# Kernel tuning notes

Hardware: AMD Instinct MI355X
Metric: run time of the kernel (lower is better)

Reference implementation:

```python
import jax, jax.numpy as jnp
import numpy as np

B, P, D, S = 1024, 200, 512, 64  # batch, num prototypes (nall), feat_dim, subdim


def setup_inputs() -> dict:
    key = jax.random.key(0)
    k1, k2, k3 = jax.random.split(key, 3)
    x = jax.random.normal(k1, (B, D), dtype=jnp.float32)
    protos = jax.random.normal(k2, (P, D), dtype=jnp.float32)
    subspaces = jax.random.normal(k3, (P, D, S), dtype=jnp.float32)
    return {"x": x, "protos": protos, "subspaces": subspaces}


def reference(x, protos, subspaces):
    # diff: [B, P, D]
    diff = x[:, None, :] - protos[None, :, :]
    # per-prototype tangent-space projectors: I - U U^T, [P, D, D]
    projectors = jnp.eye(D, dtype=subspaces.dtype) - jnp.einsum(
        'pds,pes->pde', subspaces, subspaces)
    # project diffs and take L2 norm over feature dim -> [B, P]
    proj_diff = jnp.einsum('bpd,pde->bpe', diff, projectors)
    return jnp.linalg.norm(proj_diff, ord=2, axis=-1)
```

## Files before the change

kernel.cpp:

```cpp
#include <hip/hip_runtime.h>
#include <math.h>


#define NB 1024
#define NP 200
#define ND 512
#define NS 64
#define NS5 80

#define OFF_G   0
#define OFF_C   819200
#define OFF_PN  832000
#define OFF_XN  832256
#define OFF_XB  833280
#define OFF_UB  1095424

typedef __attribute__((ext_vector_type(8))) short bf16x8;
typedef __attribute__((ext_vector_type(8))) unsigned short ushort8;
typedef __attribute__((ext_vector_type(4))) float f32x4;

__device__ __forceinline__ unsigned short f2bf(float f) {
  unsigned int u = __float_as_uint(f);
  u += 0x7fffu + ((u >> 16) & 1u);
  return (unsigned short)(u >> 16);
}

__global__ __launch_bounds__(256) void k_conv_x(const float* __restrict__ x,
                                                float* __restrict__ ws) {
  const int tid = threadIdx.x, l = tid & 63, w = tid >> 6;
  const int b = blockIdx.x * 4 + w;
  const float* src = x + (size_t)b * ND + l * 8;
  float4 v0 = *(const float4*)(src);
  float4 v1 = *(const float4*)(src + 4);
  ushort8 o;
  o[0]=f2bf(v0.x); o[1]=f2bf(v0.y); o[2]=f2bf(v0.z); o[3]=f2bf(v0.w);
  o[4]=f2bf(v1.x); o[5]=f2bf(v1.y); o[6]=f2bf(v1.z); o[7]=f2bf(v1.w);
  *(ushort8*)((unsigned short*)(ws + OFF_XB) + (size_t)b * ND + l * 8) = o;
  float s = v0.x*v0.x + v0.y*v0.y + v0.z*v0.z + v0.w*v0.w
          + v1.x*v1.x + v1.y*v1.y + v1.z*v1.z + v1.w*v1.w;
#pragma unroll
  for (int m = 1; m < 64; m <<= 1) s += __shfl_xor(s, m);
  if (l == 0) ws[OFF_XN + b] = s;
}

__global__ __launch_bounds__(256) void k_conv_u(const float* __restrict__ U,
                                                float* __restrict__ ws) {
  const int d0 = blockIdx.x * 64;
  const int p  = blockIdx.y;
  __shared__ float ts[64][68];
  const int tid = threadIdx.x;
  {
    const int dd = tid >> 4, s4 = (tid & 15) << 2;
#pragma unroll
    for (int i = 0; i < 4; ++i)
      *(float4*)&ts[dd + i*16][s4] =
          *(const float4*)(U + ((size_t)p * ND + d0 + dd + i*16) * NS + s4);
  }
  __syncthreads();
  const int s = tid >> 2, j = tid & 3;
  unsigned short* dst = (unsigned short*)(ws + OFF_UB) +
                        ((size_t)p * NS5 + s) * ND + d0 + j * 16;
  ushort8 o0, o1;
#pragma unroll
  for (int i = 0; i < 8; ++i) o0[i] = f2bf(ts[j*16 + i][s]);
#pragma unroll
  for (int i = 0; i < 8; ++i) o1[i] = f2bf(ts[j*16 + 8 + i][s]);
  *(ushort8*)dst = o0;
  *(ushort8*)(dst + 8) = o1;
}

__global__ __launch_bounds__(256) void k_conv_pz(const float* __restrict__ protos,
                                                 float* __restrict__ ws) {
  const int p = blockIdx.x, tid = threadIdx.x;
  unsigned short* ub = (unsigned short*)(ws + OFF_UB);
  float2 v = *(const float2*)(protos + (size_t)p * ND + tid * 2);
  unsigned short* d64 = ub + ((size_t)p * NS5 + 64) * ND + tid * 2;
  d64[0] = f2bf(v.x); d64[1] = f2bf(v.y);
  ushort8 z = {0,0,0,0,0,0,0,0};
#pragma unroll
  for (int i = 0; i < 4; ++i) {
    int g = tid + i * 256;
    if (g < 960)
      *(ushort8*)(ub + ((size_t)p * NS5 + 65) * ND + g * 8) = z;
  }
}

__global__ __launch_bounds__(256) void k_gram(float* __restrict__ ws) {
  const int p = blockIdx.x;
  __shared__ __align__(16) unsigned short ut[NS5 * ND];
  const int tid = threadIdx.x, l = tid & 63, w = tid >> 6;
  const int lm = l & 15, lh = l >> 4;
  const unsigned short* ub =
      (const unsigned short*)(ws + OFF_UB) + (size_t)p * NS5 * ND;
#pragma unroll
  for (int i = 0; i < 20; ++i) {
    int f = tid + i * 256;
    int r = f >> 6;
    int gd = (f & 63) ^ (r & 15);
    *(ushort8*)(ut + (size_t)f * 8) = *(const ushort8*)(ub + (size_t)r * ND + gd * 8);
  }
  __syncthreads();
  const int ntile = (w == 0) ? 6 : 5;
  for (int idx = 0; idx < ntile; ++idx) {
    int tt = (idx == 5) ? 20 : (w + 4 * idx);
    int i1 = (tt == 20) ? 4 : tt / 5;
    int i2 = (tt == 20) ? 4 : tt % 5;
    f32x4 g = {0.f, 0.f, 0.f, 0.f};
#pragma unroll
    for (int ks = 0; ks < 16; ++ks) {
      int sl = (ks * 4 + lh) ^ lm;
      bf16x8 a = *(const bf16x8*)(ut + (size_t)(i1*16 + lm) * ND + sl * 8);
      bf16x8 b = *(const bf16x8*)(ut + (size_t)(i2*16 + lm) * ND + sl * 8);
      g = __builtin_amdgcn_mfma_f32_16x16x32_bf16(a, b, g, 0, 0, 0);
    }
    int col = i2 * 16 + lm;
    int row0 = i1 * 16 + lh * 4;
    if (i1 < 4 && i2 < 4) {
#pragma unroll
      for (int q = 0; q < 4; ++q)
        ws[OFF_G + (size_t)p * 4096 + (size_t)(row0 + q) * 64 + col] = g[q];
    } else if (i1 < 4 && i2 == 4 && lm == 0) {
#pragma unroll
      for (int q = 0; q < 4; ++q) ws[OFF_C + p * 64 + row0 + q] = g[q];
    } else if (tt == 20 && l == 0) {
      ws[OFF_PN + p] = g[0];
    }
  }
}

__global__ __launch_bounds__(256) void k_main(float* __restrict__ ws,
                                              float* __restrict__ out) {
  const int p = blockIdx.y;
  const int b0 = blockIdx.x * 128;
  __shared__ __align__(16) char smem[70400];
  unsigned short* xs = (unsigned short*)smem;
  unsigned short* us = (unsigned short*)(smem + 32768);
  float* tst = (float*)smem;
  float* gs  = (float*)(smem + 53248);
  float* cs  = (float*)(smem + 69632);
  float* xps = (float*)(smem + 69888);
  const int tid = threadIdx.x, l = tid & 63, w = tid >> 6;
  const int lm = l & 15, lh = l >> 4;

#pragma unroll
  for (int it = 0; it < 4; ++it) {
    int e = tid + it * 256;
    *(float4*)(gs + e * 4) = *(const float4*)(ws + OFF_G + (size_t)p * 4096 + e * 4);
  }
  if (tid < 16)
    *(float4*)(cs + tid * 4) = *(const float4*)(ws + OFF_C + p * 64 + tid * 4);

  const unsigned short* Xb = (const unsigned short*)(ws + OFF_XB) + (size_t)b0 * ND;
  const unsigned short* Ub = (const unsigned short*)(ws + OFF_UB) + (size_t)p * NS5 * ND;

  f32x4 acc[2][5] = {};
  for (int k0 = 0; k0 < ND; k0 += 128) {
#pragma unroll
    for (int i = 0; i < 8; ++i) {
      int f = tid + i * 256;
      int r = f >> 4;
      int gd = (f & 15) ^ (r & 15);
      *(ushort8*)(xs + (size_t)f * 8) =
          *(const ushort8*)(Xb + (size_t)r * ND + k0 + gd * 8);
    }
#pragma unroll
    for (int i = 0; i < 5; ++i) {
      int f = tid + i * 256;
      int r = f >> 4;
      int gd = (f & 15) ^ (r & 15);
      *(ushort8*)(us + (size_t)f * 8) =
          *(const ushort8*)(Ub + (size_t)r * ND + k0 + gd * 8);
    }
    __syncthreads();
#pragma unroll
    for (int ks = 0; ks < 4; ++ks) {
      int gsl = ((ks * 4 + lh) ^ lm) * 8;
      bf16x8 a0 = *(const bf16x8*)(xs + (size_t)((w*2+0)*16 + lm) * 128 + gsl);
      bf16x8 a1 = *(const bf16x8*)(xs + (size_t)((w*2+1)*16 + lm) * 128 + gsl);
#pragma unroll
      for (int j = 0; j < 5; ++j) {
        bf16x8 b = *(const bf16x8*)(us + (size_t)(j*16 + lm) * 128 + gsl);
        acc[0][j] = __builtin_amdgcn_mfma_f32_16x16x32_bf16(a0, b, acc[0][j], 0, 0, 0);
        acc[1][j] = __builtin_amdgcn_mfma_f32_16x16x32_bf16(a1, b, acc[1][j], 0, 0, 0);
      }
    }
    __syncthreads();
  }

#pragma unroll
  for (int i = 0; i < 2; ++i) {
    int rbase = (w * 2 + i) * 16 + lh * 4;
#pragma unroll
    for (int j = 0; j < 5; ++j) {
      f32x4 v = acc[i][j];
      if (j < 4) {
        int col = j * 16 + lm;
        float cj = cs[col];
#pragma unroll
        for (int q = 0; q < 4; ++q)
          tst[(size_t)col * 132 + rbase + q] = v[q] - cj;
      } else if (lm == 0) {
#pragma unroll
        for (int q = 0; q < 4; ++q) xps[rbase + q] = v[q];
      }
    }
  }
  __syncthreads();

  const int tx = tid & 15, ty = tid >> 4;
  float h[8][4] = {};
#pragma unroll 4
  for (int k = 0; k < 64; ++k) {
    float4 ta = *(const float4*)(tst + k * 132 + (ty << 3));
    float4 tb = *(const float4*)(tst + k * 132 + (ty << 3) + 4);
    float4 gv = *(const float4*)(gs + k * 64 + (tx << 2));
    float tr[8] = {ta.x, ta.y, ta.z, ta.w, tb.x, tb.y, tb.z, tb.w};
    float gj[4] = {gv.x, gv.y, gv.z, gv.w};
#pragma unroll
    for (int i = 0; i < 8; ++i)
#pragma unroll
      for (int j = 0; j < 4; ++j) h[i][j] += tr[i] * gj[j];
  }

  float tgt[8], tn[8];
#pragma unroll
  for (int i = 0; i < 8; ++i) { tgt[i] = 0.f; tn[i] = 0.f; }
#pragma unroll
  for (int i = 0; i < 8; ++i)
#pragma unroll
    for (int j = 0; j < 4; ++j) {
      float tv = tst[(size_t)((tx << 2) + j) * 132 + (ty << 3) + i];
      tgt[i] += h[i][j] * tv;
      tn[i] += tv * tv;
    }
#pragma unroll
  for (int m = 1; m <= 8; m <<= 1)
#pragma unroll
    for (int i = 0; i < 8; ++i) {
      tgt[i] += __shfl_xor(tgt[i], m);
      tn[i] += __shfl_xor(tn[i], m);
    }

  if (tx == 0) {
    float pnv = ws[OFF_PN + p];
#pragma unroll
    for (int i = 0; i < 8; ++i) {
      int r = (ty << 3) + i;
      int b = b0 + r;
      float q = ws[OFF_XN + b] - 2.f * xps[r] + pnv;
      float v = q - 2.f * tn[i] + tgt[i];
      out[(size_t)b * NP + p] = sqrtf(fmaxf(v, 0.f));
    }
  }
}

extern "C" void kernel_launch(void* const* d_in, const int* in_sizes, int n_in,
                              void* d_out, int out_size, void* d_ws, size_t ws_size,
                              hipStream_t stream) {
  const float* x      = (const float*)d_in[0];
  const float* protos = (const float*)d_in[1];
  const float* U      = (const float*)d_in[2];
  float* out = (float*)d_out;
  float* ws  = (float*)d_ws;

  k_conv_x <<<dim3(NB / 4),      dim3(256), 0, stream>>>(x, ws);
  k_conv_u <<<dim3(8, NP),       dim3(256), 0, stream>>>(U, ws);
  k_conv_pz<<<dim3(NP),          dim3(256), 0, stream>>>(protos, ws);
  k_gram   <<<dim3(NP),          dim3(256), 0, stream>>>(ws);
  k_main   <<<dim3(NB / 128, NP), dim3(256), 0, stream>>>(ws, out);
}
```

Measured before the change: 145.3 us.

## Fuse preprocessing kernels and move Gram correction onto bf16 MFMA

Merges the x conversion, U transpose/conversion, proto packing and Gram computation into a single k_pre launch, so U is converted once and kept in LDS for the Gram MFMAs instead of being reread from global memory. In k_main the Gram matrix is stored as bf16 and the T·G correction runs on MFMA instead of scalar FP32 FMAs. The K-tile shrinks to 64, which cuts LDS use and should allow more resident blocks. The extra rounding of T and G to bf16 adds numerical error to the norm correction term.

```diff
diff --git a/kernel.cpp b/kernel.cpp
--- a/kernel.cpp
+++ b/kernel.cpp
@@ -8,12 +8,12 @@
 #define NS 64
 #define NS5 80
 
-#define OFF_G   0
-#define OFF_C   819200
-#define OFF_PN  832000
-#define OFF_XN  832256
-#define OFF_XB  833280
-#define OFF_UB  1095424
+#define OFF_C   0
+#define OFF_PN  12800
+#define OFF_XN  13000
+#define OFF_GB  14024
+#define OFF_XB  423624
+#define OFF_UB  685768
 
 typedef __attribute__((ext_vector_type(8))) short bf16x8;
 typedef __attribute__((ext_vector_type(8))) unsigned short ushort8;
@@ -24,82 +24,87 @@
   u += 0x7fffu + ((u >> 16) & 1u);
   return (unsigned short)(u >> 16);
 }
-
-__global__ __launch_bounds__(256) void k_conv_x(const float* __restrict__ x,
-                                                float* __restrict__ ws) {
-  const int tid = threadIdx.x, l = tid & 63, w = tid >> 6;
-  const int b = blockIdx.x * 4 + w;
-  const float* src = x + (size_t)b * ND + l * 8;
-  float4 v0 = *(const float4*)(src);
-  float4 v1 = *(const float4*)(src + 4);
-  ushort8 o;
-  o[0]=f2bf(v0.x); o[1]=f2bf(v0.y); o[2]=f2bf(v0.z); o[3]=f2bf(v0.w);
-  o[4]=f2bf(v1.x); o[5]=f2bf(v1.y); o[6]=f2bf(v1.z); o[7]=f2bf(v1.w);
-  *(ushort8*)((unsigned short*)(ws + OFF_XB) + (size_t)b * ND + l * 8) = o;
-  float s = v0.x*v0.x + v0.y*v0.y + v0.z*v0.z + v0.w*v0.w
-          + v1.x*v1.x + v1.y*v1.y + v1.z*v1.z + v1.w*v1.w;
-#pragma unroll
-  for (int m = 1; m < 64; m <<= 1) s += __shfl_xor(s, m);
-  if (l == 0) ws[OFF_XN + b] = s;
-}
-
-__global__ __launch_bounds__(256) void k_conv_u(const float* __restrict__ U,
-                                                float* __restrict__ ws) {
-  const int d0 = blockIdx.x * 64;
-  const int p  = blockIdx.y;
-  __shared__ float ts[64][68];
+__device__ __forceinline__ float bf2f(unsigned short h) {
+  return __uint_as_float(((unsigned int)h) << 16);
+}
+
+__global__ __launch_bounds__(256) void k_pre(
+    const float* __restrict__ x, const float* __restrict__ protos,
+    const float* __restrict__ U, float* __restrict__ ws)
+{
+  const int bid = blockIdx.x;
   const int tid = threadIdx.x;
+  if (bid >= NP) {
+    const int b = (bid - NP) * 32 + (tid >> 3);
+    const int cc = tid & 7;
+    const float* src = x + (size_t)b * ND + cc * 64;
+    unsigned short* dst = (unsigned short*)(ws + OFF_XB) + (size_t)b * ND + cc * 64;
+    float s = 0.f;
+#pragma unroll
+    for (int i = 0; i < 8; ++i) {
+      float4 v0 = *(const float4*)(src + i * 8);
+      float4 v1 = *(const float4*)(src + i * 8 + 4);
+      ushort8 o;
+      o[0]=f2bf(v0.x); o[1]=f2bf(v0.y); o[2]=f2bf(v0.z); o[3]=f2bf(v0.w);
+      o[4]=f2bf(v1.x); o[5]=f2bf(v1.y); o[6]=f2bf(v1.z); o[7]=f2bf(v1.w);
+      *(ushort8*)(dst + i * 8) = o;
+      s += v0.x*v0.x + v0.y*v0.y + v0.z*v0.z + v0.w*v0.w
+         + v1.x*v1.x + v1.y*v1.y + v1.z*v1.z + v1.w*v1.w;
+    }
+    s += __shfl_xor(s, 1); s += __shfl_xor(s, 2); s += __shfl_xor(s, 4);
+    if (cc == 0) ws[OFF_XN + b] = s;
+    return;
+  }
+  const int p = bid;
+  __shared__ __align__(16) unsigned short ut[NS5 * ND];
+  __shared__ float ts[32][68];
+  const int l = tid & 63, w = tid >> 6;
+  const int lm = l & 15, lh = l >> 4;
+  unsigned short* Ubg = (unsigned short*)(ws + OFF_UB) + (size_t)p * NS5 * ND;
+
+  for (int ch = 0; ch < 16; ++ch) {
+    const int d0 = ch * 32;
+    {
+      const int dd = tid >> 3, c8 = (tid & 7) * 8;
+      const float* srcu = U + ((size_t)p * ND + d0 + dd) * NS + c8;
+      *(float4*)&ts[dd][c8]     = *(const float4*)(srcu);
+      *(float4*)&ts[dd][c8 + 4] = *(const float4*)(srcu + 4);
+    }
+    __syncthreads();
+    {
+      const int s = tid >> 2, jj = tid & 3;
+      ushort8 o;
+#pragma unroll
+      for (int i = 0; i < 8; ++i) o[i] = f2bf(ts[jj * 8 + i][s]);
+      const int gd = ch * 4 + jj;
+      *(ushort8*)(ut + ((size_t)s * 64 + (gd ^ (s & 15))) * 8) = o;
+      *(ushort8*)(Ubg + (size_t)s * ND + gd * 8) = o;
+    }
+    __syncthreads();
+  }
+  if (tid < 64) {
+    const float* pr = protos + (size_t)p * ND + tid * 8;
+    float4 v0 = *(const float4*)(pr);
+    float4 v1 = *(const float4*)(pr + 4);
+    ushort8 o;
+    o[0]=f2bf(v0.x); o[1]=f2bf(v0.y); o[2]=f2bf(v0.z); o[3]=f2bf(v0.w);
+    o[4]=f2bf(v1.x); o[5]=f2bf(v1.y); o[6]=f2bf(v1.z); o[7]=f2bf(v1.w);
+    *(ushort8*)(ut + ((size_t)64 * 64 + tid) * 8) = o;
+    *(ushort8*)(Ubg + (size_t)64 * ND + tid * 8) = o;
+  }
   {
-    const int dd = tid >> 4, s4 = (tid & 15) << 2;
-#pragma unroll
-    for (int i = 0; i < 4; ++i)
-      *(float4*)&ts[dd + i*16][s4] =
-          *(const float4*)(U + ((size_t)p * ND + d0 + dd + i*16) * NS + s4);
+    ushort8 z = {0,0,0,0,0,0,0,0};
+#pragma unroll
+    for (int i = 0; i < 4; ++i) {
+      int f = tid + i * 256;
+      if (f < 960) {
+        *(ushort8*)(ut + ((size_t)65 * 64 + f) * 8) = z;
+        *(ushort8*)(Ubg + (size_t)65 * ND + f * 8) = z;
+      }
+    }
   }
   __syncthreads();
-  const int s = tid >> 2, j = tid & 3;
-  unsigned short* dst = (unsigned short*)(ws + OFF_UB) +
-                        ((size_t)p * NS5 + s) * ND + d0 + j * 16;
-  ushort8 o0, o1;
-#pragma unroll
-  for (int i = 0; i < 8; ++i) o0[i] = f2bf(ts[j*16 + i][s]);
-#pragma unroll
-  for (int i = 0; i < 8; ++i) o1[i] = f2bf(ts[j*16 + 8 + i][s]);
-  *(ushort8*)dst = o0;
-  *(ushort8*)(dst + 8) = o1;
-}
-
-__global__ __launch_bounds__(256) void k_conv_pz(const float* __restrict__ protos,
-                                                 float* __restrict__ ws) {
-  const int p = blockIdx.x, tid = threadIdx.x;
-  unsigned short* ub = (unsigned short*)(ws + OFF_UB);
-  float2 v = *(const float2*)(protos + (size_t)p * ND + tid * 2);
-  unsigned short* d64 = ub + ((size_t)p * NS5 + 64) * ND + tid * 2;
-  d64[0] = f2bf(v.x); d64[1] = f2bf(v.y);
-  ushort8 z = {0,0,0,0,0,0,0,0};
-#pragma unroll
-  for (int i = 0; i < 4; ++i) {
-    int g = tid + i * 256;
-    if (g < 960)
-      *(ushort8*)(ub + ((size_t)p * NS5 + 65) * ND + g * 8) = z;
-  }
-}
-
-__global__ __launch_bounds__(256) void k_gram(float* __restrict__ ws) {
-  const int p = blockIdx.x;
-  __shared__ __align__(16) unsigned short ut[NS5 * ND];
-  const int tid = threadIdx.x, l = tid & 63, w = tid >> 6;
-  const int lm = l & 15, lh = l >> 4;
-  const unsigned short* ub =
-      (const unsigned short*)(ws + OFF_UB) + (size_t)p * NS5 * ND;
-#pragma unroll
-  for (int i = 0; i < 20; ++i) {
-    int f = tid + i * 256;
-    int r = f >> 6;
-    int gd = (f & 63) ^ (r & 15);
-    *(ushort8*)(ut + (size_t)f * 8) = *(const ushort8*)(ub + (size_t)r * ND + gd * 8);
-  }
-  __syncthreads();
+
   const int ntile = (w == 0) ? 6 : 5;
   for (int idx = 0; idx < ntile; ++idx) {
     int tt = (idx == 5) ? 20 : (w + 4 * idx);
@@ -109,16 +114,16 @@
 #pragma unroll
     for (int ks = 0; ks < 16; ++ks) {
       int sl = (ks * 4 + lh) ^ lm;
-      bf16x8 a = *(const bf16x8*)(ut + (size_t)(i1*16 + lm) * ND + sl * 8);
-      bf16x8 b = *(const bf16x8*)(ut + (size_t)(i2*16 + lm) * ND + sl * 8);
+      bf16x8 a = *(const bf16x8*)(ut + ((size_t)(i1 * 16 + lm) * 64 + sl) * 8);
+      bf16x8 b = *(const bf16x8*)(ut + ((size_t)(i2 * 16 + lm) * 64 + sl) * 8);
       g = __builtin_amdgcn_mfma_f32_16x16x32_bf16(a, b, g, 0, 0, 0);
     }
     int col = i2 * 16 + lm;
     int row0 = i1 * 16 + lh * 4;
     if (i1 < 4 && i2 < 4) {
-#pragma unroll
-      for (int q = 0; q < 4; ++q)
-        ws[OFF_G + (size_t)p * 4096 + (size_t)(row0 + q) * 64 + col] = g[q];
+      unsigned short* Gbg = (unsigned short*)(ws + OFF_GB) + (size_t)p * 4096;
+#pragma unroll
+      for (int q = 0; q < 4; ++q) Gbg[(size_t)(row0 + q) * 64 + col] = f2bf(g[q]);
     } else if (i1 < 4 && i2 == 4 && lm == 0) {
 #pragma unroll
       for (int q = 0; q < 4; ++q) ws[OFF_C + p * 64 + row0 + q] = g[q];
@@ -129,57 +134,63 @@
 }
 
 __global__ __launch_bounds__(256) void k_main(float* __restrict__ ws,
-                                              float* __restrict__ out) {
+                                              float* __restrict__ out)
+{
   const int p = blockIdx.y;
   const int b0 = blockIdx.x * 128;
-  __shared__ __align__(16) char smem[70400];
+  __shared__ __align__(16) char smem[36608];
   unsigned short* xs = (unsigned short*)smem;
-  unsigned short* us = (unsigned short*)(smem + 32768);
-  float* tst = (float*)smem;
-  float* gs  = (float*)(smem + 53248);
-  float* cs  = (float*)(smem + 69632);
-  float* xps = (float*)(smem + 69888);
+  unsigned short* us = (unsigned short*)(smem + 16384);
+  unsigned short* tb = (unsigned short*)smem;
+  unsigned short* gs = (unsigned short*)(smem + 26624);
+  float* cs  = (float*)(smem + 35840);
+  float* xps = (float*)(smem + 36096);
   const int tid = threadIdx.x, l = tid & 63, w = tid >> 6;
   const int lm = l & 15, lh = l >> 4;
 
-#pragma unroll
-  for (int it = 0; it < 4; ++it) {
-    int e = tid + it * 256;
-    *(float4*)(gs + e * 4) = *(const float4*)(ws + OFF_G + (size_t)p * 4096 + e * 4);
-  }
-  if (tid < 16)
-    *(float4*)(cs + tid * 4) = *(const float4*)(ws + OFF_C + p * 64 + tid * 4);
+  {
+    const unsigned short* Gbg = (const unsigned short*)(ws + OFF_GB) + (size_t)p * 4096;
+#pragma unroll
+    for (int i = 0; i < 2; ++i) {
+      int f = tid + i * 256;
+      int r = f >> 3, g = f & 7;
+      *(ushort8*)(gs + (size_t)r * 72 + g * 8) =
+          *(const ushort8*)(Gbg + (size_t)r * 64 + g * 8);
+    }
+    if (tid < 16)
+      *(float4*)(cs + tid * 4) = *(const float4*)(ws + OFF_C + p * 64 + tid * 4);
+  }
 
   const unsigned short* Xb = (const unsigned short*)(ws + OFF_XB) + (size_t)b0 * ND;
   const unsigned short* Ub = (const unsigned short*)(ws + OFF_UB) + (size_t)p * NS5 * ND;
 
   f32x4 acc[2][5] = {};
-  for (int k0 = 0; k0 < ND; k0 += 128) {
-#pragma unroll
-    for (int i = 0; i < 8; ++i) {
-      int f = tid + i * 256;
-      int r = f >> 4;
-      int gd = (f & 15) ^ (r & 15);
-      *(ushort8*)(xs + (size_t)f * 8) =
-          *(const ushort8*)(Xb + (size_t)r * ND + k0 + gd * 8);
-    }
-#pragma unroll
-    for (int i = 0; i < 5; ++i) {
-      int f = tid + i * 256;
-      int r = f >> 4;
-      int gd = (f & 15) ^ (r & 15);
-      *(ushort8*)(us + (size_t)f * 8) =
-          *(const ushort8*)(Ub + (size_t)r * ND + k0 + gd * 8);
-    }
-    __syncthreads();
-#pragma unroll
-    for (int ks = 0; ks < 4; ++ks) {
-      int gsl = ((ks * 4 + lh) ^ lm) * 8;
-      bf16x8 a0 = *(const bf16x8*)(xs + (size_t)((w*2+0)*16 + lm) * 128 + gsl);
-      bf16x8 a1 = *(const bf16x8*)(xs + (size_t)((w*2+1)*16 + lm) * 128 + gsl);
+  for (int k0 = 0; k0 < ND; k0 += 64) {
+#pragma unroll
+    for (int i = 0; i < 4; ++i) {
+      int f = tid + i * 256;
+      int r = f >> 3, g = f & 7;
+      *(ushort8*)(xs + ((size_t)r * 8 + (g ^ (r & 7))) * 8) =
+          *(const ushort8*)(Xb + (size_t)r * ND + k0 + g * 8);
+    }
+#pragma unroll
+    for (int i = 0; i < 3; ++i) {
+      int f = tid + i * 256;
+      if (f < 640) {
+        int r = f >> 3, g = f & 7;
+        *(ushort8*)(us + ((size_t)r * 8 + (g ^ (r & 7))) * 8) =
+            *(const ushort8*)(Ub + (size_t)r * ND + k0 + g * 8);
+      }
+    }
+    __syncthreads();
+#pragma unroll
+    for (int ks = 0; ks < 2; ++ks) {
+      int slot = (ks * 4 + lh) ^ (lm & 7);
+      bf16x8 a0 = *(const bf16x8*)(xs + (((size_t)((w*2+0)*16 + lm)) * 8 + slot) * 8);
+      bf16x8 a1 = *(const bf16x8*)(xs + (((size_t)((w*2+1)*16 + lm)) * 8 + slot) * 8);
 #pragma unroll
       for (int j = 0; j < 5; ++j) {
-        bf16x8 b = *(const bf16x8*)(us + (size_t)(j*16 + lm) * 128 + gsl);
+        bf16x8 b = *(const bf16x8*)(us + (((size_t)(j*16 + lm)) * 8 + slot) * 8);
         acc[0][j] = __builtin_amdgcn_mfma_f32_16x16x32_bf16(a0, b, acc[0][j], 0, 0, 0);
         acc[1][j] = __builtin_amdgcn_mfma_f32_16x16x32_bf16(a1, b, acc[1][j], 0, 0, 0);
       }
@@ -187,6 +198,7 @@
     __syncthreads();
   }
 
+  float tn[2][4] = {};
 #pragma unroll
   for (int i = 0; i < 2; ++i) {
     int rbase = (w * 2 + i) * 16 + lh * 4;
@@ -197,8 +209,11 @@
         int col = j * 16 + lm;
         float cj = cs[col];
 #pragma unroll
-        for (int q = 0; q < 4; ++q)
-          tst[(size_t)col * 132 + rbase + q] = v[q] - cj;
+        for (int q = 0; q < 4; ++q) {
+          float t = v[q] - cj;
+          tn[i][q] += t * t;
+          tb[(size_t)(rbase + q) * 72 + col] = f2bf(t);
+        }
       } else if (lm == 0) {
 #pragma unroll
         for (int q = 0; q < 4; ++q) xps[rbase + q] = v[q];
@@ -207,49 +222,51 @@
   }
   __syncthreads();
 
-  const int tx = tid & 15, ty = tid >> 4;
-  float h[8][4] = {};
-#pragma unroll 4
-  for (int k = 0; k < 64; ++k) {
-    float4 ta = *(const float4*)(tst + k * 132 + (ty << 3));
-    float4 tb = *(const float4*)(tst + k * 132 + (ty << 3) + 4);
-    float4 gv = *(const float4*)(gs + k * 64 + (tx << 2));
-    float tr[8] = {ta.x, ta.y, ta.z, ta.w, tb.x, tb.y, tb.z, tb.w};
-    float gj[4] = {gv.x, gv.y, gv.z, gv.w};
-#pragma unroll
-    for (int i = 0; i < 8; ++i)
-#pragma unroll
-      for (int j = 0; j < 4; ++j) h[i][j] += tr[i] * gj[j];
-  }
-
-  float tgt[8], tn[8];
-#pragma unroll
-  for (int i = 0; i < 8; ++i) { tgt[i] = 0.f; tn[i] = 0.f; }
-#pragma unroll
-  for (int i = 0; i < 8; ++i)
+  f32x4 acc2[2][4] = {};
+#pragma unroll
+  for (int ks = 0; ks < 2; ++ks) {
+#pragma unroll
+    for (int i = 0; i < 2; ++i) {
+      bf16x8 a = *(const bf16x8*)(tb + (size_t)((w*2+i)*16 + lm) * 72 + ks*32 + lh*8);
+#pragma unroll
+      for (int j = 0; j < 4; ++j) {
+        bf16x8 b = *(const bf16x8*)(gs + (size_t)(j*16 + lm) * 72 + ks*32 + lh*8);
+        acc2[i][j] = __builtin_amdgcn_mfma_f32_16x16x32_bf16(a, b, acc2[i][j], 0, 0, 0);
+      }
+    }
+  }
+
+  const float pnv = ws[OFF_PN + p];
+#pragma unroll
+  for (int i = 0; i < 2; ++i) {
+    int rbase = (w * 2 + i) * 16 + lh * 4;
+    float tgt[4] = {0.f, 0.f, 0.f, 0.f};
 #pragma unroll
     for (int j = 0; j < 4; ++j) {
-      float tv = tst[(size_t)((tx << 2) + j) * 132 + (ty << 3) + i];
-      tgt[i] += h[i][j] * tv;
-      tn[i] += tv * tv;
-    }
-#pragma unroll
-  for (int m = 1; m <= 8; m <<= 1)
-#pragma unroll
-    for (int i = 0; i < 8; ++i) {
-      tgt[i] += __shfl_xor(tgt[i], m);
-      tn[i] += __shfl_xor(tn[i], m);
-    }
-
-  if (tx == 0) {
-    float pnv = ws[OFF_PN + p];
-#pragma unroll
-    for (int i = 0; i < 8; ++i) {
-      int r = (ty << 3) + i;
-      int b = b0 + r;
-      float q = ws[OFF_XN + b] - 2.f * xps[r] + pnv;
-      float v = q - 2.f * tn[i] + tgt[i];
-      out[(size_t)b * NP + p] = sqrtf(fmaxf(v, 0.f));
+      int col = j * 16 + lm;
+#pragma unroll
+      for (int q = 0; q < 4; ++q)
+        tgt[q] += acc2[i][j][q] * bf2f(tb[(size_t)(rbase + q) * 72 + col]);
+    }
+#pragma unroll
+    for (int q = 0; q < 4; ++q) {
+      float ta = tgt[q], tname = tn[i][q];
+#pragma unroll
+      for (int m = 1; m <= 8; m <<= 1) {
+        ta += __shfl_xor(ta, m);
+        tname += __shfl_xor(tname, m);
+      }
+      tgt[q] = ta; tn[i][q] = tname;
+    }
+    if (lm == 0) {
+#pragma unroll
+      for (int q = 0; q < 4; ++q) {
+        int r = rbase + q;
+        int bb = b0 + r;
+        float qq = ws[OFF_XN + bb] - 2.f * xps[r] + pnv;
+        float v = qq - 2.f * tn[i][q] + tgt[q];
+        out[(size_t)bb * NP + p] = sqrtf(fmaxf(v, 0.f));
+      }
     }
   }
 }
@@ -263,9 +280,6 @@
   float* out = (float*)d_out;
   float* ws  = (float*)d_ws;
 
-  k_conv_x <<<dim3(NB / 4),      dim3(256), 0, stream>>>(x, ws);
-  k_conv_u <<<dim3(8, NP),       dim3(256), 0, stream>>>(U, ws);
-  k_conv_pz<<<dim3(NP),          dim3(256), 0, stream>>>(protos, ws);
-  k_gram   <<<dim3(NP),          dim3(256), 0, stream>>>(ws);
-  k_main   <<<dim3(NB / 128, NP), dim3(256), 0, stream>>>(ws, out);
-}
+  k_pre <<<dim3(NP + NB / 32), dim3(256), 0, stream>>>(x, protos, U, ws);
+  k_main<<<dim3(NB / 128, NP), dim3(256), 0, stream>>>(ws, out);
+}
```

Result: faster. 133.7 us (-8.0%).
